# Performance work log

Measured on AMD Instinct MI355X. Metric: run time of the kernel, lower is better.

## Reference

```python
import jax, jax.numpy as jnp
import numpy as np

EPS = 1e-8          # EPSILON in source
THRESH = 0.5        # state.match_threshold
MIN_RADIUS = 0.05   # meaningful-observation threshold

B, T, H, D, N = 4, 4096, 2048, 256, 32768
Hq = H // 4


def setup_inputs() -> dict:
    key = jax.random.key(0)
    ks = jax.random.split(key, 10)
    s = 0.02
    return {
        "hidden": jax.random.normal(ks[0], (B, T, H), jnp.float32),
        "beliefs": jax.random.normal(ks[1], (N, D), jnp.float32),
        "active_mask": jax.random.bernoulli(ks[2], 0.5, (N,)),
        "W_obs": jax.random.normal(ks[3], (D, H), jnp.float32) * s,
        "W_g1": jax.random.normal(ks[4], (Hq, H), jnp.float32) * s,
        "b_g1": jnp.zeros((Hq,), jnp.float32),
        "W_g2": jax.random.normal(ks[5], (1, Hq), jnp.float32) * s,
        "b_g2": jnp.full((1,), -2.0, jnp.float32),  # nn.init.constant_(bias, -2.0)
        "W_p1": jax.random.normal(ks[6], (Hq, H), jnp.float32) * s,
        "b_p1": jnp.zeros((Hq,), jnp.float32),
        "W_p2": jax.random.normal(ks[7], (1, Hq), jnp.float32) * s,
        "b_p2": jnp.zeros((1,), jnp.float32),
    }


def reference(hidden, beliefs, active_mask, W_obs, W_g1, b_g1, W_g2, b_g2,
              W_p1, b_p1, W_p2, b_p2):
    # --- projections (torch Linear: y = x @ W.T + b) ---
    obs = jnp.einsum("bth,dh->btd", hidden, W_obs)                       # [B,T,D]
    gate = jax.nn.sigmoid(
        jnp.einsum("btq,oq->bto",
                   jax.nn.relu(jnp.einsum("bth,qh->btq", hidden, W_g1) + b_g1),
                   W_g2) + b_g2)                                          # [B,T,1]
    prec = jax.nn.softplus(
        jnp.einsum("btq,oq->bto",
                   jax.nn.relu(jnp.einsum("bth,qh->btq", hidden, W_p1) + b_p1),
                   W_p2) + b_p2)                                          # [B,T,1]
    gated_prec = gate * prec

    obs_mean = obs.mean(axis=0)          # [T,D]
    prec_mean = gated_prec.mean(axis=0)  # [T,1]
    # F.normalize: x / max(||x||, eps)
    obs_angles = obs_mean / jnp.maximum(
        jnp.linalg.norm(obs_mean, axis=-1, keepdims=True), EPS)
    obs_beliefs = obs_angles * prec_mean  # [T,D] radius = precision

    # --- cosine-similarity 1-NN match against active beliefs ---
    b_radii = jnp.clip(jnp.linalg.norm(beliefs, axis=-1), EPS, None)     # [N]
    b_angles = beliefs / b_radii[:, None]
    o_radii_c = jnp.clip(jnp.linalg.norm(obs_beliefs, axis=-1), EPS, None)
    o_angles = obs_beliefs / o_radii_c[:, None]
    sims = jnp.einsum("td,nd->tn", o_angles, b_angles)                    # [T,N]
    sims_masked = jnp.where(active_mask[None, :], sims, -jnp.inf)
    any_active = jnp.any(active_mask)
    best_sims = jnp.where(any_active, jnp.max(sims_masked, axis=-1), 0.0)  # [T]
    best_global = jnp.where(any_active, jnp.argmax(sims_masked, axis=-1), -1)

    obs_radii = jnp.linalg.norm(obs_beliefs, axis=-1)  # unclamped
    meaningful = obs_radii > MIN_RADIUS
    matched = meaningful & (best_sims > THRESH) & any_active
    slots = jnp.where(matched, best_global, -1)          # matched slot or -1 (new)
    sims_out = jnp.where(matched, best_sims, 0.0)
    return obs_beliefs, sims_out, slots, meaningful
```

## Files before the change

### kernel.cpp

```cpp
#include <hip/hip_runtime.h>
#include <hip/hip_bf16.h>
#include <math.h>

#define TB 4
#define TT 4096
#define HH 2048
#define DD 256
#define NN 32768
#define HQ 512
#define MM (TB*TT)

typedef __attribute__((ext_vector_type(8))) short bf16x8;
typedef __attribute__((ext_vector_type(8))) _Float16 f16x8;
typedef __attribute__((ext_vector_type(4))) float f32x4;

__device__ inline unsigned short f2bf(float x){
  __hip_bfloat16 h = __float2bfloat16(x);
  return *reinterpret_cast<unsigned short*>(&h);
}

__device__ inline unsigned short f2h(float x){
  _Float16 h = (_Float16)x;
  unsigned short u; __builtin_memcpy(&u, &h, 2); return u;
}

__device__ inline bf16x8 as_bf16x8(uint4 u){ bf16x8 r; __builtin_memcpy(&r,&u,16); return r; }

__device__ __forceinline__ void gload_ldsv(const void* g, void* l){
  __builtin_amdgcn_global_load_lds(
      (const __attribute__((address_space(1))) unsigned int*)g,
      (__attribute__((address_space(3))) unsigned int*)l, 16, 0, 0);
}

__global__ __launch_bounds__(256) void k_mean(const float* __restrict__ h,
    unsigned short* __restrict__ hmb){
  const size_t i = (size_t)blockIdx.x*256 + threadIdx.x;
  const size_t TH4 = (size_t)TT*HH/4;
  const float4* p = (const float4*)h;
  float4 v0 = p[i], v1 = p[i+TH4], v2 = p[i+2*TH4], v3 = p[i+3*TH4];
  float4 m;
  m.x = 0.25f*(v0.x+v1.x+v2.x+v3.x);
  m.y = 0.25f*(v0.y+v1.y+v2.y+v3.y);
  m.z = 0.25f*(v0.z+v1.z+v2.z+v3.z);
  m.w = 0.25f*(v0.w+v1.w+v2.w+v3.w);
  ushort4 o; o.x = f2bf(m.x); o.y = f2bf(m.y); o.z = f2bf(m.z); o.w = f2bf(m.w);
  *(ushort4*)(hmb + i*4) = o;
}

__global__ __launch_bounds__(256) void k_cvt_w(const float* __restrict__ Wg1,
    const float* __restrict__ Wp1, unsigned short* __restrict__ Wsw){
  const int id = blockIdx.x*256 + threadIdx.x;
  const int n = id >> 8;
  const int cg = id & 255;
  const int k = cg*8;
  const int kc = cg >> 2;
  const int c8 = cg & 3;
  const float* src = (n < HQ) ? (Wg1 + (size_t)n*HH + k) : (Wp1 + (size_t)(n-HQ)*HH + k);
  float4 v0 = *(const float4*)src;
  float4 v1 = *(const float4*)(src + 4);
  unsigned short o[8] = {f2h(v0.x),f2h(v0.y),f2h(v0.z),f2h(v0.w),
                         f2h(v1.x),f2h(v1.y),f2h(v1.z),f2h(v1.w)};
  const int nb = n >> 8, r = n & 255;
  const int s = (r & 3) ^ ((r >> 2) & 3);
  unsigned short* dst = Wsw + ((size_t)(nb*64 + kc))*8192 + r*32 + ((c8 ^ s) << 3);
  __builtin_memcpy(dst, o, 16);
}

__global__ __launch_bounds__(256) void k_cvt_wobs(const float* __restrict__ W,
    unsigned short* __restrict__ Wb){
  const int idx4 = blockIdx.x*256 + threadIdx.x;
  float4 v = *(const float4*)(W + (size_t)idx4*4);
  ushort4 o; o.x = f2bf(v.x); o.y = f2bf(v.y); o.z = f2bf(v.z); o.w = f2bf(v.w);
  *(ushort4*)(Wb + (size_t)idx4*4) = o;
}

__global__ __launch_bounds__(256) void k_obs(const unsigned short* __restrict__ A,
    const unsigned short* __restrict__ Bw, float* __restrict__ C){
  const int n0 = blockIdx.x*128, m0 = blockIdx.y*128;
  const int tid = threadIdx.x;
  const int w = tid>>6, lane = tid&63, lr = lane&15, q = lane>>4;
  __shared__ __align__(16) unsigned short Bs[128][40];
  f32x4 acc[2][8] = {};
  for (int k0 = 0; k0 < HH; k0 += 32){
    __syncthreads();
    #pragma unroll
    for (int ii = 0; ii < 2; ii++){
      int idx = tid + ii*256;
      int row = idx >> 2, c8 = (idx & 3)*8;
      *(uint4*)&Bs[row][c8] = *(const uint4*)(Bw + (size_t)(n0+row)*HH + k0 + c8);
    }
    bf16x8 a[2];
    #pragma unroll
    for (int i = 0; i < 2; i++)
      a[i] = as_bf16x8(*(const uint4*)(A + (size_t)(m0 + w*32 + i*16 + lr)*HH + k0 + q*8));
    __syncthreads();
    #pragma unroll
    for (int j = 0; j < 8; j++){
      bf16x8 b = as_bf16x8(*(const uint4*)&Bs[j*16 + lr][q*8]);
      #pragma unroll
      for (int i = 0; i < 2; i++)
        acc[i][j] = __builtin_amdgcn_mfma_f32_16x16x32_bf16(a[i], b, acc[i][j], 0, 0, 0);
    }
  }
  #pragma unroll
  for (int i = 0; i < 2; i++)
    #pragma unroll
    for (int j = 0; j < 8; j++)
      #pragma unroll
      for (int r = 0; r < 4; r++)
        C[(size_t)(m0 + w*32 + i*16 + q*4 + r)*DD + n0 + j*16 + lr] = acc[i][j][r];
}

__global__ __launch_bounds__(256, 2) void k_gp(const float* __restrict__ A,
    const unsigned short* __restrict__ Wsw,
    const float* __restrict__ bg1, const float* __restrict__ bp1,
    const float* __restrict__ Wg2, const float* __restrict__ Wp2,
    float* __restrict__ z1, float* __restrict__ z2){
  const int bid = blockIdx.x;
  const int nb = (bid >> 3) & 3;
  const int my = (bid & 7) + ((bid >> 5) << 3);
  const int m0 = my*128;
  const int tid = threadIdx.x;
  const int w = tid>>6, lane = tid&63, lr = lane&15, q = lane>>4;
  __shared__ __align__(16) unsigned short Ws[2][8192];
  __shared__ __align__(16) float As[2][4096];
  f32x4 acc[2][16] = {};

  const unsigned short* wt = Wsw + (size_t)nb*64*8192 + w*2048 + lane*8;
  const int rpB = lr*32 + ((q ^ ((lr & 3) ^ ((lr >> 2) & 3))) << 3);
  const int sr8 = lane >> 3;
  const int sc  = (lane & 7) ^ sr8;
  const float* asrc = A + (size_t)(m0 + w*32 + sr8)*HH + sc*4;

  #pragma unroll
  for (int i = 0; i < 4; i++){
    gload_ldsv(wt + i*512, &Ws[0][w*2048 + i*512]);
    gload_ldsv(asrc + (size_t)i*8*HH, &As[0][(w*32 + i*8)*32]);
  }
  __syncthreads();

  for (int t = 0; t < 64; t++){
    const int cur = t & 1;
    if (t < 63){
      #pragma unroll
      for (int i = 0; i < 4; i++){
        gload_ldsv(wt + (size_t)(t+1)*8192 + i*512, &Ws[cur^1][w*2048 + i*512]);
        gload_ldsv(asrc + (size_t)i*8*HH + (t+1)*32, &As[cur^1][(w*32 + i*8)*32]);
      }
    }
    const float* At = As[cur];
    f16x8 ah[2], al[2];
    #pragma unroll
    for (int i = 0; i < 2; i++){
      const int tr = w*32 + i*16 + lr;
      const int px = lr & 7;
      float4 fa = *(const float4*)&At[tr*32 + (((2*q)   ^ px) << 2)];
      float4 fb = *(const float4*)&At[tr*32 + (((2*q+1) ^ px) << 2)];
      float av[8] = {fa.x,fa.y,fa.z,fa.w, fb.x,fb.y,fb.z,fb.w};
      #pragma unroll
      for (int e = 0; e < 8; e++){
        _Float16 h = (_Float16)av[e];
        ah[i][e] = h; al[i][e] = (_Float16)(av[e] - (float)h);
      }
    }
    const unsigned short* Wc = Ws[cur];
    __builtin_amdgcn_s_setprio(1);
    #pragma unroll
    for (int j = 0; j < 16; j++){
      f16x8 bh;
      __builtin_memcpy(&bh, Wc + j*512 + rpB, 16);
      acc[0][j] = __builtin_amdgcn_mfma_f32_16x16x32_f16(ah[0], bh, acc[0][j], 0, 0, 0);
      acc[1][j] = __builtin_amdgcn_mfma_f32_16x16x32_f16(ah[1], bh, acc[1][j], 0, 0, 0);
      acc[0][j] = __builtin_amdgcn_mfma_f32_16x16x32_f16(al[0], bh, acc[0][j], 0, 0, 0);
      acc[1][j] = __builtin_amdgcn_mfma_f32_16x16x32_f16(al[1], bh, acc[1][j], 0, 0, 0);
    }
    __builtin_amdgcn_s_setprio(0);
    __syncthreads();
  }

  const bool isP = (nb >= 2);
  const float* b1 = isP ? bp1 : bg1;
  const float* w2 = isP ? Wp2 : Wg2;
  float* zt = isP ? z2 : z1;
  const int nbl = nb*256 - (isP ? HQ : 0);
  float s[2][4] = {};
  #pragma unroll
  for (int j = 0; j < 16; j++){
    const int n = nbl + j*16 + lr;
    const float bb = b1[n], ww = w2[n];
    #pragma unroll
    for (int i = 0; i < 2; i++)
      #pragma unroll
      for (int r = 0; r < 4; r++)
        s[i][r] += fmaxf(acc[i][j][r] + bb, 0.f) * ww;
  }
  #pragma unroll
  for (int mk = 1; mk < 16; mk <<= 1)
    #pragma unroll
    for (int i = 0; i < 2; i++)
      #pragma unroll
      for (int r = 0; r < 4; r++)
        s[i][r] += __shfl_xor(s[i][r], mk);
  if (lr == 0){
    #pragma unroll
    for (int i = 0; i < 2; i++)
      #pragma unroll
      for (int r = 0; r < 4; r++)
        atomicAdd(&zt[m0 + w*32 + i*16 + q*4 + r], s[i][r]);
  }
}

__global__ __launch_bounds__(256) void k_obs_fin(const float* __restrict__ obs_mean,
    const float* __restrict__ z1, const float* __restrict__ z2,
    const float* __restrict__ bg2, const float* __restrict__ bp2,
    float* __restrict__ out0, float* __restrict__ out3,
    float* __restrict__ obs_radii, unsigned short* __restrict__ obf){
  const int w = threadIdx.x >> 6, lane = threadIdx.x & 63;
  const int t = blockIdx.x*4 + w;
  float pm = 0.f;
  if (lane < TB){
    float a = z1[lane*TT + t] + bg2[0];
    float b = z2[lane*TT + t] + bp2[0];
    float gate = 1.f/(1.f + expf(-a));
    float sp = (b > 0.f) ? (b + log1pf(expf(-b))) : log1pf(expf(b));
    pm = gate * sp;
  }
  #pragma unroll
  for (int m = 1; m < 4; m <<= 1) pm += __shfl_xor(pm, m);
  pm = __shfl(pm, 0) * 0.25f;
  float4 x = *(const float4*)(obs_mean + (size_t)t*DD + lane*4);
  float ss = x.x*x.x + x.y*x.y + x.z*x.z + x.w*x.w;
  #pragma unroll
  for (int m = 1; m < 64; m <<= 1) ss += __shfl_xor(ss, m);
  const float nrm = sqrtf(ss);
  const float sc = pm / fmaxf(nrm, 1e-8f);
  float4 ob = {x.x*sc, x.y*sc, x.z*sc, x.w*sc};
  *(float4*)(out0 + (size_t)t*DD + lane*4) = ob;
  float s2 = ob.x*ob.x + ob.y*ob.y + ob.z*ob.z + ob.w*ob.w;
  #pragma unroll
  for (int m = 1; m < 64; m <<= 1) s2 += __shfl_xor(s2, m);
  const float r2 = sqrtf(s2);
  if (lane == 0){
    obs_radii[t] = r2;
    out3[t] = (r2 > 0.05f) ? 1.f : 0.f;
  }
  const float inv2 = 1.f / fmaxf(r2, 1e-8f);
  ushort4 o = {f2bf(ob.x*inv2), f2bf(ob.y*inv2), f2bf(ob.z*inv2), f2bf(ob.w*inv2)};
  *(ushort4*)(obf + (size_t)t*DD + lane*4) = o;
}

__global__ __launch_bounds__(256) void k_beliefs(const float* __restrict__ bel,
    unsigned short* __restrict__ bbf){
  const int n = (blockIdx.x*256 + threadIdx.x) >> 6;
  const int lane = threadIdx.x & 63;
  const float4 v = *(const float4*)(bel + (size_t)n*DD + lane*4);
  float s = v.x*v.x + v.y*v.y + v.z*v.z + v.w*v.w;
  #pragma unroll
  for (int m = 1; m < 64; m <<= 1) s += __shfl_xor(s, m);
  const float inv = 1.f / fmaxf(sqrtf(s), 1e-8f);
  ushort4 o;
  o.x = f2bf(v.x*inv); o.y = f2bf(v.y*inv); o.z = f2bf(v.z*inv); o.w = f2bf(v.w*inv);
  *(ushort4*)(bbf + (size_t)n*DD + lane*4) = o;
}

__global__ __launch_bounds__(256) void k_any(const unsigned char* __restrict__ mask,
    int* __restrict__ flag){
  const int i = blockIdx.x*256 + threadIdx.x;
  const int any = (mask[i] != 0) ? 1 : 0;
  if (__ballot(any)){
    if ((threadIdx.x & 63) == 0) atomicOr(flag, 1);
  }
}

__global__ __launch_bounds__(256) void k_sims(const unsigned short* __restrict__ obf,
    const unsigned short* __restrict__ bbf, const unsigned char* __restrict__ mask,
    float* __restrict__ pmax, int* __restrict__ pidx){
  const int bid = blockIdx.x;
  const int rest = bid >> 3;
  const int ns = (bid & 7) + ((rest >> 5) << 3);
  const int t0 = (rest & 31) * 128;
  const int nbase0 = ns * (NN/32);
  const int tid = threadIdx.x;
  const int w = tid >> 6, lane = tid & 63;
  const int lr = lane & 15, q = lane >> 4;
  __shared__ __align__(16) unsigned short bt[2][64*256];
  const int srow = lane >> 5;
  const int sp   = lane & 31;

  #pragma unroll
  for (int i = 0; i < 8; i++){
    const int rb = (i*4 + w)*2;
    const int row = rb + srow;
    const unsigned short* src = bbf + (size_t)(nbase0 + row)*DD + ((sp ^ (row & 31)) << 3);
    gload_ldsv(src, &bt[0][(i*4 + w)*512]);
  }
  bf16x8 afr[2][8];
  #pragma unroll
  for (int i = 0; i < 2; i++){
    const unsigned short* ap = obf + (size_t)(t0 + w*32 + i*16 + lr)*DD + q*8;
    #pragma unroll
    for (int ks = 0; ks < 8; ks++)
      afr[i][ks] = as_bf16x8(*(const uint4*)(ap + ks*32));
  }
  __syncthreads();

  float vmax[2][4] = {{-INFINITY,-INFINITY,-INFINITY,-INFINITY},
                      {-INFINITY,-INFINITY,-INFINITY,-INFINITY}};
  int   vidx[2][4] = {{-1,-1,-1,-1},{-1,-1,-1,-1}};
  int cur = 0;
  for (int it = 0; it < (NN/32)/64; it++){
    const int nb = nbase0 + it*64;
    if (it < (NN/32)/64 - 1){
      const int nbn = nb + 64;
      #pragma unroll
      for (int i = 0; i < 8; i++){
        const int rb = (i*4 + w)*2;
        const int row = rb + srow;
        const unsigned short* src = bbf + (size_t)(nbn + row)*DD + ((sp ^ (row & 31)) << 3);
        gload_ldsv(src, &bt[cur^1][(i*4 + w)*512]);
      }
    }
    const unsigned short* btc = bt[cur];
    #pragma unroll
    for (int sub = 0; sub < 4; sub++){
      const int rowi = sub*16 + lr;
      const bool act = (mask[nb + rowi] != 0);
      const unsigned short* bp = btc + rowi*256;
      const int rx = rowi & 31;
      f32x4 acc[2] = {{0.f,0.f,0.f,0.f},{0.f,0.f,0.f,0.f}};
      #pragma unroll
      for (int ks = 0; ks < 8; ks++){
        const int p = (q + ks*4) ^ rx;
        bf16x8 bfr = as_bf16x8(*(const uint4*)(bp + p*8));
        acc[0] = __builtin_amdgcn_mfma_f32_16x16x32_bf16(afr[0][ks], bfr, acc[0], 0, 0, 0);
        acc[1] = __builtin_amdgcn_mfma_f32_16x16x32_bf16(afr[1][ks], bfr, acc[1], 0, 0, 0);
      }
      if (act){
        const int n = nb + rowi;
        #pragma unroll
        for (int i = 0; i < 2; i++)
          #pragma unroll
          for (int r = 0; r < 4; r++)
            if (acc[i][r] > vmax[i][r]){ vmax[i][r] = acc[i][r]; vidx[i][r] = n; }
      }
    }
    __syncthreads();
    cur ^= 1;
  }
  #pragma unroll
  for (int mk = 1; mk < 16; mk <<= 1){
    #pragma unroll
    for (int i = 0; i < 2; i++)
      #pragma unroll
      for (int r = 0; r < 4; r++){
        float om = __shfl_xor(vmax[i][r], mk);
        int   oi = __shfl_xor(vidx[i][r], mk);
        if (om > vmax[i][r] || (om == vmax[i][r] && (unsigned)oi < (unsigned)vidx[i][r])){
          vmax[i][r] = om; vidx[i][r] = oi;
        }
      }
  }
  if (lr == 0){
    #pragma unroll
    for (int i = 0; i < 2; i++)
      #pragma unroll
      for (int r = 0; r < 4; r++){
        const int t = t0 + w*32 + i*16 + q*4 + r;
        pmax[ns*TT + t] = vmax[i][r];
        pidx[ns*TT + t] = vidx[i][r];
      }
  }
}

__global__ __launch_bounds__(256) void k_combine(const float* __restrict__ pmax,
    const int* __restrict__ pidx, const float* __restrict__ obs_radii,
    const int* __restrict__ flag, float* __restrict__ out1, float* __restrict__ out2){
  const int t = blockIdx.x*256 + threadIdx.x;
  float best = -INFINITY; int bi = -1;
  #pragma unroll
  for (int s = 0; s < 32; s++){
    float m = pmax[s*TT + t];
    if (m > best){ best = m; bi = pidx[s*TT + t]; }
  }
  const bool anyA = (flag[0] != 0);
  const bool mf = obs_radii[t] > 0.05f;
  const bool matched = mf && anyA && (best > 0.5f);
  out1[t] = matched ? best : 0.f;
  out2[t] = matched ? (float)bi : -1.f;
}

extern "C" void kernel_launch(void* const* d_in, const int* in_sizes, int n_in,
                              void* d_out, int out_size, void* d_ws, size_t ws_size,
                              hipStream_t stream) {
  const float* hidden = (const float*)d_in[0];
  const float* beliefs = (const float*)d_in[1];
  const unsigned char* amask = (const unsigned char*)d_in[2];
  const float* W_obs = (const float*)d_in[3];
  const float* W_g1 = (const float*)d_in[4];
  const float* b_g1 = (const float*)d_in[5];
  const float* W_g2 = (const float*)d_in[6];
  const float* b_g2 = (const float*)d_in[7];
  const float* W_p1 = (const float*)d_in[8];
  const float* b_p1 = (const float*)d_in[9];
  const float* W_p2 = (const float*)d_in[10];
  const float* b_p2 = (const float*)d_in[11];

  char* ws = (char*)d_ws;
  const size_t HMB_OFF  = 0;
  const size_t WSW_OFF  = 16777216;
  const size_t WOB_OFF  = 20971520;
  const size_t OM_OFF   = 22020096;
  const size_t Z1_OFF   = 26214400;
  const size_t Z2_OFF   = 26279936;
  const size_t FLAG_OFF = 26345472;
  const size_t RAD_OFF  = 26345728;
  const size_t OBF_OFF  = 26362112;
  const size_t BBF_OFF  = 28459264;
  const size_t PMAX_OFF = 45236480;
  const size_t PIDX_OFF = 45760768;

  unsigned short* hmb = (unsigned short*)(ws + HMB_OFF);
  unsigned short* Wsw = (unsigned short*)(ws + WSW_OFF);
  unsigned short* wob = (unsigned short*)(ws + WOB_OFF);
  float* om  = (float*)(ws + OM_OFF);
  float* z1  = (float*)(ws + Z1_OFF);
  float* z2  = (float*)(ws + Z2_OFF);
  int*   flg = (int*)(ws + FLAG_OFF);
  float* rad = (float*)(ws + RAD_OFF);
  unsigned short* obf = (unsigned short*)(ws + OBF_OFF);
  unsigned short* bbf = (unsigned short*)(ws + BBF_OFF);
  float* pmax = (float*)(ws + PMAX_OFF);
  int*   pidx = (int*)(ws + PIDX_OFF);

  float* out0 = (float*)d_out;
  float* out1 = out0 + (size_t)TT*DD;
  float* out2 = out1 + TT;
  float* out3 = out2 + TT;

  hipMemsetAsync(ws + Z1_OFF, 0, 2*MM*sizeof(float) + 256, stream);

  k_mean    <<<TT*HH/4/256, 256, 0, stream>>>(hidden, hmb);
  k_cvt_w   <<<(1024*HH/8)/256, 256, 0, stream>>>(W_g1, W_p1, Wsw);
  k_cvt_wobs<<<(DD*HH/4)/256, 256, 0, stream>>>(W_obs, wob);
  k_obs     <<<dim3(DD/128, TT/128), 256, 0, stream>>>(hmb, wob, om);
  k_gp      <<<512, 256, 0, stream>>>(hidden, Wsw, b_g1, b_p1, W_g2, W_p2, z1, z2);
  k_obs_fin <<<TT/4, 256, 0, stream>>>(om, z1, z2, b_g2, b_p2, out0, out3, rad, obf);
  k_beliefs <<<NN/4, 256, 0, stream>>>(beliefs, bbf);
  k_any     <<<NN/256, 256, 0, stream>>>(amask, flg);
  k_sims    <<<1024, 256, 0, stream>>>(obf, bbf, amask, pmax, pidx);
  k_combine <<<TT/256, 256, 0, stream>>>(pmax, pidx, rad, flg, out1, out2);
}
```

Measured before the change: 511.3 us.

## Fuse prep kernels, pipeline obs GEMM via LDS, shrink sims tiles with LDS mask

Merges the weight conversion, W_obs conversion, belief normalization and any-active check into one k_prep launch, which cuts per-launch overhead. Rewrites k_obs so both A and B tiles are loaded into double-buffered, swizzled LDS with async global-to-LDS loads, letting the next tile's loads overlap the current MFMAs. In k_sims the belief tile is halved to 32 rows per stage, and the mask slice is staged in LDS instead of read from global on every sub-tile. MFMA sections also get raised wave priority via s_setprio. The smaller sims tile lowers LDS use, which may allow more resident blocks, but it doubles the number of loop iterations and barriers.

```diff
diff --git a/kernel.cpp b/kernel.cpp
--- a/kernel.cpp
+++ b/kernel.cpp
@@ -47,31 +47,57 @@
   *(ushort4*)(hmb + i*4) = o;
 }
 
-__global__ __launch_bounds__(256) void k_cvt_w(const float* __restrict__ Wg1,
-    const float* __restrict__ Wp1, unsigned short* __restrict__ Wsw){
-  const int id = blockIdx.x*256 + threadIdx.x;
-  const int n = id >> 8;
-  const int cg = id & 255;
-  const int k = cg*8;
-  const int kc = cg >> 2;
-  const int c8 = cg & 3;
-  const float* src = (n < HQ) ? (Wg1 + (size_t)n*HH + k) : (Wp1 + (size_t)(n-HQ)*HH + k);
-  float4 v0 = *(const float4*)src;
-  float4 v1 = *(const float4*)(src + 4);
-  unsigned short o[8] = {f2h(v0.x),f2h(v0.y),f2h(v0.z),f2h(v0.w),
-                         f2h(v1.x),f2h(v1.y),f2h(v1.z),f2h(v1.w)};
-  const int nb = n >> 8, r = n & 255;
-  const int s = (r & 3) ^ ((r >> 2) & 3);
-  unsigned short* dst = Wsw + ((size_t)(nb*64 + kc))*8192 + r*32 + ((c8 ^ s) << 3);
-  __builtin_memcpy(dst, o, 16);
-}
-
-__global__ __launch_bounds__(256) void k_cvt_wobs(const float* __restrict__ W,
-    unsigned short* __restrict__ Wb){
-  const int idx4 = blockIdx.x*256 + threadIdx.x;
-  float4 v = *(const float4*)(W + (size_t)idx4*4);
-  ushort4 o; o.x = f2bf(v.x); o.y = f2bf(v.y); o.z = f2bf(v.z); o.w = f2bf(v.w);
-  *(ushort4*)(Wb + (size_t)idx4*4) = o;
+#define PREP_CVTW 1024
+#define PREP_WOBS 512
+#define PREP_BEL  8192
+#define PREP_ANY  128
+__global__ __launch_bounds__(256) void k_prep(
+    const float* __restrict__ Wg1, const float* __restrict__ Wp1,
+    unsigned short* __restrict__ Wsw,
+    const float* __restrict__ Wobs, unsigned short* __restrict__ wob,
+    const float* __restrict__ bel, unsigned short* __restrict__ bbf,
+    const unsigned char* __restrict__ mask, int* __restrict__ flag){
+  const int b = blockIdx.x;
+  if (b < PREP_CVTW){
+    const int id = b*256 + threadIdx.x;
+    const int n = id >> 8;
+    const int cg = id & 255;
+    const int k = cg*8;
+    const int kc = cg >> 2;
+    const int c8 = cg & 3;
+    const float* src = (n < HQ) ? (Wg1 + (size_t)n*HH + k) : (Wp1 + (size_t)(n-HQ)*HH + k);
+    float4 v0 = *(const float4*)src;
+    float4 v1 = *(const float4*)(src + 4);
+    unsigned short o[8] = {f2h(v0.x),f2h(v0.y),f2h(v0.z),f2h(v0.w),
+                           f2h(v1.x),f2h(v1.y),f2h(v1.z),f2h(v1.w)};
+    const int nb = n >> 8, r = n & 255;
+    const int s = (r & 3) ^ ((r >> 2) & 3);
+    unsigned short* dst = Wsw + ((size_t)(nb*64 + kc))*8192 + r*32 + ((c8 ^ s) << 3);
+    __builtin_memcpy(dst, o, 16);
+  } else if (b < PREP_CVTW + PREP_WOBS){
+    const int idx4 = (b - PREP_CVTW)*256 + threadIdx.x;
+    float4 v = *(const float4*)(Wobs + (size_t)idx4*4);
+    ushort4 o; o.x = f2bf(v.x); o.y = f2bf(v.y); o.z = f2bf(v.z); o.w = f2bf(v.w);
+    *(ushort4*)(wob + (size_t)idx4*4) = o;
+  } else if (b < PREP_CVTW + PREP_WOBS + PREP_BEL){
+    const int bb = b - (PREP_CVTW + PREP_WOBS);
+    const int n = (bb*256 + threadIdx.x) >> 6;
+    const int lane = threadIdx.x & 63;
+    const float4 v = *(const float4*)(bel + (size_t)n*DD + lane*4);
+    float s = v.x*v.x + v.y*v.y + v.z*v.z + v.w*v.w;
+    #pragma unroll
+    for (int m = 1; m < 64; m <<= 1) s += __shfl_xor(s, m);
+    const float inv = 1.f / fmaxf(sqrtf(s), 1e-8f);
+    ushort4 o;
+    o.x = f2bf(v.x*inv); o.y = f2bf(v.y*inv); o.z = f2bf(v.z*inv); o.w = f2bf(v.w*inv);
+    *(ushort4*)(bbf + (size_t)n*DD + lane*4) = o;
+  } else {
+    const int i = (b - (PREP_CVTW + PREP_WOBS + PREP_BEL))*256 + threadIdx.x;
+    const int any = (mask[i] != 0) ? 1 : 0;
+    if (__ballot(any)){
+      if ((threadIdx.x & 63) == 0) atomicOr(flag, 1);
+    }
+  }
 }
 
 __global__ __launch_bounds__(256) void k_obs(const unsigned short* __restrict__ A,
@@ -79,28 +105,43 @@
   const int n0 = blockIdx.x*128, m0 = blockIdx.y*128;
   const int tid = threadIdx.x;
   const int w = tid>>6, lane = tid&63, lr = lane&15, q = lane>>4;
-  __shared__ __align__(16) unsigned short Bs[128][40];
+  __shared__ __align__(16) unsigned short As[2][4096];
+  __shared__ __align__(16) unsigned short Bs[2][4096];
   f32x4 acc[2][8] = {};
-  for (int k0 = 0; k0 < HH; k0 += 32){
+  const int srow = lane >> 2;
+  const int sch  = (lane & 3) ^ (srow & 3);
+  const unsigned short* asrc = A  + (size_t)(m0 + w*32 + srow)*HH + sch*8;
+  const unsigned short* bsrc = Bw + (size_t)(n0 + w*32 + srow)*HH + sch*8;
+
+  #pragma unroll
+  for (int i = 0; i < 2; i++){
+    gload_ldsv(asrc + (size_t)i*16*HH, &As[0][(w*32 + i*16)*32]);
+    gload_ldsv(bsrc + (size_t)i*16*HH, &Bs[0][(w*32 + i*16)*32]);
+  }
+  __syncthreads();
+
+  for (int t = 0; t < 64; t++){
+    const int cur = t & 1;
+    if (t < 63){
+      const int ko = (t+1)*32;
+      #pragma unroll
+      for (int i = 0; i < 2; i++){
+        gload_ldsv(asrc + (size_t)i*16*HH + ko, &As[cur^1][(w*32 + i*16)*32]);
+        gload_ldsv(bsrc + (size_t)i*16*HH + ko, &Bs[cur^1][(w*32 + i*16)*32]);
+      }
+    }
+    bf16x8 a[2];
+    #pragma unroll
+    for (int i = 0; i < 2; i++)
+      a[i] = as_bf16x8(*(const uint4*)&As[cur][(w*32 + i*16 + lr)*32 + ((q ^ (lr&3))<<3)]);
+    #pragma unroll
+    for (int j = 0; j < 8; j++){
+      bf16x8 bb = as_bf16x8(*(const uint4*)&Bs[cur][(j*16 + lr)*32 + ((q ^ (lr&3))<<3)]);
+      #pragma unroll
+      for (int i = 0; i < 2; i++)
+        acc[i][j] = __builtin_amdgcn_mfma_f32_16x16x32_bf16(a[i], bb, acc[i][j], 0, 0, 0);
+    }
     __syncthreads();
-    #pragma unroll
-    for (int ii = 0; ii < 2; ii++){
-      int idx = tid + ii*256;
-      int row = idx >> 2, c8 = (idx & 3)*8;
-      *(uint4*)&Bs[row][c8] = *(const uint4*)(Bw + (size_t)(n0+row)*HH + k0 + c8);
-    }
-    bf16x8 a[2];
-    #pragma unroll
-    for (int i = 0; i < 2; i++)
-      a[i] = as_bf16x8(*(const uint4*)(A + (size_t)(m0 + w*32 + i*16 + lr)*HH + k0 + q*8));
-    __syncthreads();
-    #pragma unroll
-    for (int j = 0; j < 8; j++){
-      bf16x8 b = as_bf16x8(*(const uint4*)&Bs[j*16 + lr][q*8]);
-      #pragma unroll
-      for (int i = 0; i < 2; i++)
-        acc[i][j] = __builtin_amdgcn_mfma_f32_16x16x32_bf16(a[i], b, acc[i][j], 0, 0, 0);
-    }
   }
   #pragma unroll
   for (int i = 0; i < 2; i++)
@@ -249,29 +290,6 @@
   *(ushort4*)(obf + (size_t)t*DD + lane*4) = o;
 }
 
-__global__ __launch_bounds__(256) void k_beliefs(const float* __restrict__ bel,
-    unsigned short* __restrict__ bbf){
-  const int n = (blockIdx.x*256 + threadIdx.x) >> 6;
-  const int lane = threadIdx.x & 63;
-  const float4 v = *(const float4*)(bel + (size_t)n*DD + lane*4);
-  float s = v.x*v.x + v.y*v.y + v.z*v.z + v.w*v.w;
-  #pragma unroll
-  for (int m = 1; m < 64; m <<= 1) s += __shfl_xor(s, m);
-  const float inv = 1.f / fmaxf(sqrtf(s), 1e-8f);
-  ushort4 o;
-  o.x = f2bf(v.x*inv); o.y = f2bf(v.y*inv); o.z = f2bf(v.z*inv); o.w = f2bf(v.w*inv);
-  *(ushort4*)(bbf + (size_t)n*DD + lane*4) = o;
-}
-
-__global__ __launch_bounds__(256) void k_any(const unsigned char* __restrict__ mask,
-    int* __restrict__ flag){
-  const int i = blockIdx.x*256 + threadIdx.x;
-  const int any = (mask[i] != 0) ? 1 : 0;
-  if (__ballot(any)){
-    if ((threadIdx.x & 63) == 0) atomicOr(flag, 1);
-  }
-}
-
 __global__ __launch_bounds__(256) void k_sims(const unsigned short* __restrict__ obf,
     const unsigned short* __restrict__ bbf, const unsigned char* __restrict__ mask,
     float* __restrict__ pmax, int* __restrict__ pidx){
@@ -283,14 +301,16 @@
   const int tid = threadIdx.x;
   const int w = tid >> 6, lane = tid & 63;
   const int lr = lane & 15, q = lane >> 4;
-  __shared__ __align__(16) unsigned short bt[2][64*256];
+  __shared__ __align__(16) unsigned short bt[2][32*256];
+  __shared__ __align__(16) unsigned char am[1024];
   const int srow = lane >> 5;
   const int sp   = lane & 31;
 
-  #pragma unroll
-  for (int i = 0; i < 8; i++){
-    const int rb = (i*4 + w)*2;
-    const int row = rb + srow;
+  ((unsigned int*)am)[tid] = ((const unsigned int*)(mask + nbase0))[tid];
+
+  #pragma unroll
+  for (int i = 0; i < 4; i++){
+    const int row = (i*4 + w)*2 + srow;
     const unsigned short* src = bbf + (size_t)(nbase0 + row)*DD + ((sp ^ (row & 31)) << 3);
     gload_ldsv(src, &bt[0][(i*4 + w)*512]);
   }
@@ -308,35 +328,34 @@
                       {-INFINITY,-INFINITY,-INFINITY,-INFINITY}};
   int   vidx[2][4] = {{-1,-1,-1,-1},{-1,-1,-1,-1}};
   int cur = 0;
-  for (int it = 0; it < (NN/32)/64; it++){
-    const int nb = nbase0 + it*64;
-    if (it < (NN/32)/64 - 1){
-      const int nbn = nb + 64;
-      #pragma unroll
-      for (int i = 0; i < 8; i++){
-        const int rb = (i*4 + w)*2;
-        const int row = rb + srow;
-        const unsigned short* src = bbf + (size_t)(nbn + row)*DD + ((sp ^ (row & 31)) << 3);
+  for (int it = 0; it < 32; it++){
+    const int nl = it*32;
+    if (it < 31){
+      #pragma unroll
+      for (int i = 0; i < 4; i++){
+        const int row = (i*4 + w)*2 + srow;
+        const unsigned short* src = bbf + (size_t)(nbase0 + nl + 32 + row)*DD + ((sp ^ (row & 31)) << 3);
         gload_ldsv(src, &bt[cur^1][(i*4 + w)*512]);
       }
     }
     const unsigned short* btc = bt[cur];
     #pragma unroll
-    for (int sub = 0; sub < 4; sub++){
+    for (int sub = 0; sub < 2; sub++){
       const int rowi = sub*16 + lr;
-      const bool act = (mask[nb + rowi] != 0);
+      const bool act = (am[nl + rowi] != 0);
       const unsigned short* bp = btc + rowi*256;
-      const int rx = rowi & 31;
       f32x4 acc[2] = {{0.f,0.f,0.f,0.f},{0.f,0.f,0.f,0.f}};
+      __builtin_amdgcn_s_setprio(1);
       #pragma unroll
       for (int ks = 0; ks < 8; ks++){
-        const int p = (q + ks*4) ^ rx;
-        bf16x8 bfr = as_bf16x8(*(const uint4*)(bp + p*8));
+        const int p = (q + ks*4) ^ rowi;
+        bf16x8 bfr = as_bf16x8(*(const uint4*)(bp + (p & 31)*8));
         acc[0] = __builtin_amdgcn_mfma_f32_16x16x32_bf16(afr[0][ks], bfr, acc[0], 0, 0, 0);
         acc[1] = __builtin_amdgcn_mfma_f32_16x16x32_bf16(afr[1][ks], bfr, acc[1], 0, 0, 0);
       }
+      __builtin_amdgcn_s_setprio(0);
       if (act){
-        const int n = nb + rowi;
+        const int n = nbase0 + nl + rowi;
         #pragma unroll
         for (int i = 0; i < 2; i++)
           #pragma unroll
@@ -439,14 +458,12 @@
 
   hipMemsetAsync(ws + Z1_OFF, 0, 2*MM*sizeof(float) + 256, stream);
 
+  k_prep    <<<PREP_CVTW + PREP_WOBS + PREP_BEL + PREP_ANY, 256, 0, stream>>>(
+                W_g1, W_p1, Wsw, W_obs, wob, beliefs, bbf, amask, flg);
   k_mean    <<<TT*HH/4/256, 256, 0, stream>>>(hidden, hmb);
-  k_cvt_w   <<<(1024*HH/8)/256, 256, 0, stream>>>(W_g1, W_p1, Wsw);
-  k_cvt_wobs<<<(DD*HH/4)/256, 256, 0, stream>>>(W_obs, wob);
   k_obs     <<<dim3(DD/128, TT/128), 256, 0, stream>>>(hmb, wob, om);
   k_gp      <<<512, 256, 0, stream>>>(hidden, Wsw, b_g1, b_p1, W_g2, W_p2, z1, z2);
   k_obs_fin <<<TT/4, 256, 0, stream>>>(om, z1, z2, b_g2, b_p2, out0, out3, rad, obf);
-  k_beliefs <<<NN/4, 256, 0, stream>>>(beliefs, bbf);
-  k_any     <<<NN/256, 256, 0, stream>>>(amask, flg);
   k_sims    <<<1024, 256, 0, stream>>>(obf, bbf, amask, pmax, pidx);
   k_combine <<<TT/256, 256, 0, stream>>>(pmax, pidx, rad, flg, out1, out2);
 }
```

After: 502.1 us. About the same (-1.8%).
